# Kernel tuning notes

Hardware: AMD Instinct MI355X
Metric: run time of the kernel (lower is better)

## Reference

```python
import jax, jax.numpy as jnp
import numpy as np

N_NODES = 100000
N_EDGES = 3200000
# (out_dim, in_dim) for the 4 BayesianLinear layers: mlp1 = [5->16, 16->32], mlp2 = [35->16, 16->1]
LAYER_DIMS = [(16, 5), (32, 16), (16, 35), (1, 16)]


def setup_inputs() -> dict:
    key = jax.random.key(0)
    ks = iter(jax.random.split(key, 32))
    inp = {}
    inp["x"] = jax.random.normal(next(ks), (N_NODES, 3), jnp.float32)
    inp["edge_attr"] = jax.random.normal(next(ks), (N_EDGES, 2), jnp.float32)
    inp["edge_index"] = jax.random.randint(next(ks), (2, N_EDGES), 0, N_NODES, dtype=jnp.int64)
    for li, (o, i) in enumerate(LAYER_DIMS, 1):
        inp[f"l{li}_wmu"] = jax.random.normal(next(ks), (o, i), jnp.float32) * 0.1
        inp[f"l{li}_wrho"] = jax.random.normal(next(ks), (o, i), jnp.float32) * 0.1 - 5.0
        inp[f"l{li}_bmu"] = jax.random.normal(next(ks), (o,), jnp.float32) * 0.1
        inp[f"l{li}_brho"] = jax.random.normal(next(ks), (o,), jnp.float32) * 0.1 - 5.0
        inp[f"l{li}_eps_w"] = jax.random.normal(next(ks), (o, i), jnp.float32)
        inp[f"l{li}_eps_b"] = jax.random.normal(next(ks), (o,), jnp.float32)
    return inp


def _bayes_linear(h, wmu, wrho, bmu, brho, eps_w, eps_b):
    # sampled weight: W = mu + softplus(rho) * eps  (blitz BayesianLinear)
    W = wmu + jax.nn.softplus(wrho) * eps_w          # [out, in]
    b = bmu + jax.nn.softplus(brho) * eps_b          # [out]
    return h @ W.T + b


def _igconv(x, edge_index, edge_attr, p1, p2, p3, p4):
    src, dst = edge_index[0], edge_index[1]          # x_j = x[src], aggregate at dst
    x_j = x[src]                                     # [E, 3] irregular gather
    m = jnp.concatenate([x_j, edge_attr], axis=1)    # [E, 5]
    m = jax.nn.relu(_bayes_linear(m, *p1))           # [E, 16]
    m = jax.nn.relu(_bayes_linear(m, *p2))           # [E, 32]
    agg = jax.ops.segment_max(m, dst, num_segments=x.shape[0])  # [N, 32]
    agg = jnp.where(jnp.isneginf(agg), 0.0, agg)     # nodes with no in-edges -> 0
    h = jnp.concatenate([x, agg], axis=1)            # [N, 35]
    h = jax.nn.relu(_bayes_linear(h, *p3))           # [N, 16]
    comb = jax.nn.sigmoid(_bayes_linear(h, *p4))     # [N, 1]
    return jnp.concatenate([x[:, :2], comb], axis=1) # [N, 3]


def reference(x, edge_attr, edge_index,
              l1_wmu, l1_wrho, l1_bmu, l1_brho, l1_eps_w, l1_eps_b,
              l2_wmu, l2_wrho, l2_bmu, l2_brho, l2_eps_w, l2_eps_b,
              l3_wmu, l3_wrho, l3_bmu, l3_brho, l3_eps_w, l3_eps_b,
              l4_wmu, l4_wrho, l4_bmu, l4_brho, l4_eps_w, l4_eps_b):
    p1 = (l1_wmu, l1_wrho, l1_bmu, l1_brho, l1_eps_w, l1_eps_b)
    p2 = (l2_wmu, l2_wrho, l2_bmu, l2_brho, l2_eps_w, l2_eps_b)
    p3 = (l3_wmu, l3_wrho, l3_bmu, l3_brho, l3_eps_w, l3_eps_b)
    p4 = (l4_wmu, l4_wrho, l4_bmu, l4_brho, l4_eps_w, l4_eps_b)
    h = x
    for _ in range(3):  # three stacked applications of the same IGConv
        h = _igconv(h, edge_index, edge_attr, p1, p2, p3, p4)
    return h
```

## Files before the change

kernel.cpp:

```cpp
#include <hip/hip_runtime.h>
#include <math.h>

#define WTOT  1233
#define PKOFS 1280
#define PKTOT 352

typedef __fp16 h2 __attribute__((ext_vector_type(2)));
typedef __fp16 f16x8 __attribute__((ext_vector_type(8)));
typedef float f32x16 __attribute__((ext_vector_type(16)));

struct ERec { int s; int d; unsigned int ea; };

__device__ __forceinline__ h2 u2h(unsigned int u) { return __builtin_bit_cast(h2, u); }
__device__ __forceinline__ unsigned int h2u(h2 h) { return __builtin_bit_cast(unsigned int, h); }
#define DOT2(a, b, c) __builtin_amdgcn_fdot2((a), (b), (c), false)

__device__ __forceinline__ float softplus_f(float x) {
  return fmaxf(x, 0.f) + log1pf(expf(-fabsf(x)));
}

struct PrepArgs {
  const float* wmu[4]; const float* wrho[4]; const float* epsw[4];
  const float* bmu[4]; const float* brho[4]; const float* epsb[4];
  float* out; int* bucketCur; int nbuck;
};

__global__ void prep_all_kernel(PrepArgs a) {
  const int wsz[4] = {80, 512, 560, 16};
  const int wof[4] = {0, 96, 640, 1216};
  const int bsz[4] = {16, 32, 16, 1};
  const int bof[4] = {80, 608, 1200, 1232};
  float* wg = a.out;
  int tid = threadIdx.x;
  if (tid < a.nbuck) a.bucketCur[tid] = 0;
#pragma unroll
  for (int l = 0; l < 4; l++) {
    for (int i = tid; i < wsz[l]; i += 1024)
      wg[wof[l] + i] = a.wmu[l][i] + softplus_f(a.wrho[l][i]) * a.epsw[l][i];
    for (int i = tid; i < bsz[l]; i += 1024)
      wg[bof[l] + i] = a.bmu[l][i] + softplus_f(a.brho[l][i]) * a.epsb[l][i];
  }
  __syncthreads();
  unsigned int* wp = (unsigned int*)(wg + PKOFS);
  int t = tid;
  if (t < 16) {
    wp[t]      = h2u(h2{(__fp16)wg[t * 5 + 0], (__fp16)wg[t * 5 + 1]});
    wp[16 + t] = h2u(h2{(__fp16)wg[t * 5 + 2], (__fp16)0.f});
    wp[32 + t] = h2u(h2{(__fp16)wg[t * 5 + 3], (__fp16)wg[t * 5 + 4]});
    ((float*)wp)[304 + t] = wg[80 + t];
  }
  if (t < 32) {
    ((float*)wp)[320 + t] = wg[608 + t];
    for (int j = 0; j < 8; j++)
      wp[48 + t * 8 + j] =
          h2u(h2{(__fp16)wg[96 + t * 16 + 2 * j], (__fp16)wg[96 + t * 16 + 2 * j + 1]});
  }
}

__global__ __launch_bounds__(1024) void bhist_kernel(const int* __restrict__ dst,
                                                     int* __restrict__ bucketCur,
                                                     int E, int NBUCK) {
  __shared__ int h[1024];
  int tid = threadIdx.x;
  for (int i = tid; i < NBUCK; i += 1024) h[i] = 0;
  __syncthreads();
  int base = blockIdx.x * 8192;
#pragma unroll
  for (int r = 0; r < 8; r++) {
    int e = base + r * 1024 + tid;
    if (e < E) atomicAdd(&h[dst[e] >> 7], 1);
  }
  __syncthreads();
  for (int i = tid; i < NBUCK; i += 1024) {
    int c = h[i];
    if (c) atomicAdd(&bucketCur[i], c);
  }
}

__global__ __launch_bounds__(1024) void scanBk_kernel(int* __restrict__ bucketCur,
                                                      int* __restrict__ bucketOff,
                                                      int NBUCK) {
  __shared__ int wsum[16];
  __shared__ int woff[16];
  int tid = threadIdx.x, lane = tid & 63, wid = tid >> 6;
  int v = (tid < NBUCK) ? bucketCur[tid] : 0;
  int x = v;
#pragma unroll
  for (int off = 1; off < 64; off <<= 1) {
    int t = __shfl_up(x, off, 64);
    if (lane >= off) x += t;
  }
  if (lane == 63) wsum[wid] = x;
  __syncthreads();
  if (wid == 0) {
    int s = (lane < 16) ? wsum[lane] : 0;
#pragma unroll
    for (int off = 1; off < 16; off <<= 1) {
      int t = __shfl_up(s, off, 64);
      if (lane >= off) s += t;
    }
    if (lane < 16) woff[lane] = s - wsum[lane];
  }
  __syncthreads();
  int excl = woff[wid] + x - v;
  if (tid < NBUCK) {
    bucketOff[tid] = excl;
    bucketCur[tid] = excl;
    if (tid == NBUCK - 1) bucketOff[NBUCK] = excl + v;
  }
}

__global__ __launch_bounds__(1024) void part_kernel(
    const int* __restrict__ src, const int* __restrict__ dst,
    const float2* __restrict__ ea, int* __restrict__ bucketCur,
    ERec* __restrict__ brec, int E, int NBUCK) {
  __shared__ int h[1024];
  int tid = threadIdx.x;
  for (int i = tid; i < NBUCK; i += 1024) h[i] = 0;
  __syncthreads();
  int base = blockIdx.x * 8192;
  int d[8], s[8];
  unsigned int a[8];
  bool v[8];
#pragma unroll
  for (int j = 0; j < 8; j++) {
    int e = base + j * 1024 + tid;
    v[j] = e < E;
    if (v[j]) {
      d[j] = dst[e];
      s[j] = src[e];
      float2 t = ea[e];
      a[j] = h2u(__builtin_amdgcn_cvt_pkrtz(t.x, t.y));
      atomicAdd(&h[d[j] >> 7], 1);
    }
  }
  __syncthreads();
  for (int i = tid; i < NBUCK; i += 1024) {
    int c = h[i];
    h[i] = c ? atomicAdd(&bucketCur[i], c) : 0;
  }
  __syncthreads();
#pragma unroll
  for (int j = 0; j < 8; j++) {
    if (v[j]) {
      int pos = atomicAdd(&h[d[j] >> 7], 1);
      ERec t; t.s = s[j]; t.d = d[j]; t.ea = a[j];
      brec[pos] = t;
    }
  }
}

__global__ __launch_bounds__(256) void deg_kernel(const ERec* __restrict__ brec,
                                                  const int* __restrict__ bucketOff,
                                                  int* __restrict__ deg, int N) {
  __shared__ int cnt[128];
  int b = blockIdx.x, tid = threadIdx.x;
  if (tid < 128) cnt[tid] = 0;
  __syncthreads();
  int e0 = bucketOff[b], e1 = bucketOff[b + 1];
  for (int i = e0 + tid; i < e1; i += 256) atomicAdd(&cnt[brec[i].d & 127], 1);
  __syncthreads();
  int node = b * 128 + tid;
  if (tid < 128 && node < N) deg[node] = cnt[tid];
}

__global__ void scanA_kernel(const int* __restrict__ deg, int* __restrict__ part, int n) {
  __shared__ int ws[16];
  int tid = threadIdx.x;
  int i = blockIdx.x * 1024 + tid;
  int v = 0;
  if (i < n) v = (deg[i] + 3) & ~3;
#pragma unroll
  for (int off = 32; off >= 1; off >>= 1) v += __shfl_down(v, off, 64);
  if ((tid & 63) == 0) ws[tid >> 6] = v;
  __syncthreads();
  if (tid == 0) {
    int s = 0;
#pragma unroll
    for (int k = 0; k < 16; k++) s += ws[k];
    part[blockIdx.x] = s;
  }
}

__global__ void scanB_kernel(int* __restrict__ part, int P, int* __restrict__ etot) {
  int lane = threadIdx.x;
  int carry = 0;
  for (int base = 0; base < P; base += 64) {
    int i = base + lane;
    int v = (i < P) ? part[i] : 0;
    int x = v;
#pragma unroll
    for (int off = 1; off < 64; off <<= 1) {
      int t = __shfl_up(x, off, 64);
      if (lane >= off) x += t;
    }
    if (i < P) part[i] = carry + x - v;
    carry += __shfl(x, 63, 64);
  }
  if (lane == 0) *etot = carry;
}

__global__ void scanC_kernel(const int* __restrict__ deg, const int* __restrict__ part,
                             int* __restrict__ cursor, int n) {
  __shared__ int wsum[16];
  __shared__ int woff[16];
  int tid = threadIdx.x, lane = tid & 63, wid = tid >> 6;
  int i = blockIdx.x * 1024 + tid;
  int v = 0;
  if (i < n) v = (deg[i] + 3) & ~3;
  int x = v;
#pragma unroll
  for (int off = 1; off < 64; off <<= 1) {
    int t = __shfl_up(x, off, 64);
    if (lane >= off) x += t;
  }
  if (lane == 63) wsum[wid] = x;
  __syncthreads();
  if (wid == 0) {
    int s = (lane < 16) ? wsum[lane] : 0;
#pragma unroll
    for (int off = 1; off < 16; off <<= 1) {
      int t = __shfl_up(s, off, 64);
      if (lane >= off) s += t;
    }
    if (lane < 16) woff[lane] = s - wsum[lane];
  }
  __syncthreads();
  if (i < n) cursor[i] = part[blockIdx.x] + woff[wid] + x - v;
}

__global__ __launch_bounds__(256) void scat_kernel(
    const ERec* __restrict__ brec, const int* __restrict__ bucketOff,
    const int* __restrict__ cursor, ERec* __restrict__ erec, int N) {
  __shared__ int lcur[128];
  int b = blockIdx.x, tid = threadIdx.x;
  int node = b * 128 + tid;
  if (tid < 128) lcur[tid] = (node < N) ? cursor[node] : 0;
  __syncthreads();
  int e0 = bucketOff[b], e1 = bucketOff[b + 1];
  for (int i = e0 + tid; i < e1; i += 256) {
    ERec t = brec[i];
    int pos = atomicAdd(&lcur[t.d & 127], 1);
    erec[pos] = t;
  }
  __syncthreads();
  if (tid < 128 && node < N) {
    int cur = cursor[node];
    int endR = lcur[tid];
    int endP = cur + ((endR - cur + 3) & ~3);
    if (endR > cur) {
      ERec rep = erec[cur];
      for (int k = endR; k < endP; k++) erec[k] = rep;
    }
  }
}

__global__ void xpack_kernel(const float* __restrict__ x, uint2* __restrict__ xpk,
                             unsigned int* __restrict__ agg32, int n) {
  int i = blockIdx.x * blockDim.x + threadIdx.x;
  if (i < n) {
    h2 a = __builtin_amdgcn_cvt_pkrtz(x[3 * i], x[3 * i + 1]);
    h2 b = __builtin_amdgcn_cvt_pkrtz(x[3 * i + 2], 0.f);
    xpk[i] = make_uint2(h2u(a), h2u(b));
    uint4 z = make_uint4(0u, 0u, 0u, 0u);
    uint4* ap = (uint4*)(agg32 + (size_t)i * 32);
#pragma unroll
    for (int k = 0; k < 8; k++) ap[k] = z;
    if (i == 0) {
      uint4* as = (uint4*)(agg32 + (size_t)n * 32);
#pragma unroll
      for (int k = 0; k < 8; k++) as[k] = z;
    }
  }
}

__global__ __launch_bounds__(256) void edge_kernel(
    const uint2* __restrict__ xpk, const ERec* __restrict__ erec,
    unsigned int* __restrict__ agg32,
    const float* __restrict__ wg, const int* __restrict__ pEtot, int N) {
  __shared__ __align__(16) unsigned int lds[4][64][12];
  const unsigned int* wp = (const unsigned int*)(wg + PKOFS);
  const float* bf = (const float*)wp;
  const int Etot = *pEtot;
  if (blockIdx.x * 256 >= Etot) return;
  const int tid = threadIdx.x;
  const int lane = tid & 63;
  const int wslot = tid >> 6;
  const int e = blockIdx.x * 256 + tid;

  bool vld = e < Etot;
  ERec r;
  r.s = 0; r.d = N; r.ea = 0u;
  if (vld) r = erec[e];
  int d = r.d;
  uint2 xs = xpk[r.s];

  h2 p01 = u2h(xs.x), p2v = u2h(xs.y), pea = u2h(r.ea);
  unsigned int m1[8];
#pragma unroll
  for (int p = 0; p < 8; p++) {
    const int oA = 2 * p, oB = 2 * p + 1;
    float sA = DOT2(p01, u2h(wp[oA]),
                DOT2(p2v, u2h(wp[16 + oA]),
                DOT2(pea, u2h(wp[32 + oA]), bf[304 + oA])));
    float sB = DOT2(p01, u2h(wp[oB]),
                DOT2(p2v, u2h(wp[16 + oB]),
                DOT2(pea, u2h(wp[32 + oB]), bf[304 + oB])));
    m1[p] = h2u(__builtin_amdgcn_cvt_pkrtz(fmaxf(sA, 0.f), fmaxf(sB, 0.f)));
  }

  uint4* rowp = (uint4*)&lds[wslot][lane][0];
  rowp[0] = make_uint4(m1[0], m1[1], m1[2], m1[3]);
  rowp[1] = make_uint4(m1[4], m1[5], m1[6], m1[7]);
  asm volatile("s_waitcnt lgkmcnt(0)" ::: "memory");
  __builtin_amdgcn_sched_barrier(0);

  const int col = lane & 31;
  const int h = lane >> 5;
  f16x8 bfrag = __builtin_bit_cast(f16x8, *(const uint4*)&wp[48 + col * 8 + 4 * h]);
  float bias = bf[320 + col];
  f32x16 cini;
#pragma unroll
  for (int i = 0; i < 16; i++) cini[i] = bias;

  f16x8 a0 = __builtin_bit_cast(f16x8, *(const uint4*)&lds[wslot][col][4 * h]);
  f16x8 a1 = __builtin_bit_cast(f16x8, *(const uint4*)&lds[wslot][32 + col][4 * h]);
  f32x16 acc0 = __builtin_amdgcn_mfma_f32_32x32x16_f16(a0, bfrag, cini, 0, 0, 0);
  f32x16 acc1 = __builtin_amdgcn_mfma_f32_32x32x16_f16(a1, bfrag, cini, 0, 0, 0);

  float bm[2][4];
#pragma unroll
  for (int q = 0; q < 4; q++) {
    bm[0][q] = fmaxf(fmaxf(acc0[4 * q], acc0[4 * q + 1]),
                     fmaxf(acc0[4 * q + 2], fmaxf(acc0[4 * q + 3], 0.f)));
    bm[1][q] = fmaxf(fmaxf(acc1[4 * q], acc1[4 * q + 1]),
                     fmaxf(acc1[4 * q + 2], fmaxf(acc1[4 * q + 3], 0.f)));
  }

  int dp4 = __shfl_up(d, 4, 64);
  bool isHead = ((lane & 3) == 0) && (lane == 0 || d != dp4);
  unsigned long long hm = __ballot(isHead);

  unsigned long long rem = hm;
  while (rem) {
    int a = (int)__builtin_ctzll(rem);
    rem &= rem - 1;
    int b = rem ? (int)__builtin_ctzll(rem) : 64;
    int rd = __shfl(d, a, 64);
    int A = a >> 2, B = b >> 2;
    float mx = 0.f;
#pragma unroll
    for (int g = 0; g < 2; g++) {
#pragma unroll
      for (int q = 0; q < 4; q++) {
        int blk = 8 * g + 2 * q + h;
        bool in = (blk >= A) && (blk < B);
        mx = fmaxf(mx, in ? bm[g][q] : 0.f);
      }
    }
    mx = fmaxf(mx, __shfl_xor(mx, 32, 64));
    if (lane < 32 && rd < N)
      atomicMax(agg32 + (size_t)rd * 32 + col, __float_as_uint(mx));
  }
}

__global__ __launch_bounds__(256) void node_kernel(
    const float* __restrict__ x, const float* __restrict__ cin,
    float* __restrict__ cout, uint2* __restrict__ xpk,
    float* __restrict__ outFinal, unsigned int* __restrict__ agg32,
    const float* __restrict__ wg, int n) {
  int nid = blockIdx.x * blockDim.x + threadIdx.x;
  if (nid >= n) return;
  uint4* ap = (uint4*)(agg32 + (size_t)nid * 32);
  uint4 q[8];
#pragma unroll
  for (int i = 0; i < 8; i++) q[i] = ap[i];
  uint4 z = make_uint4(0u, 0u, 0u, 0u);
#pragma unroll
  for (int i = 0; i < 8; i++) ap[i] = z;
  float av[32];
#pragma unroll
  for (int i = 0; i < 8; i++) {
    av[4 * i + 0] = __uint_as_float(q[i].x);
    av[4 * i + 1] = __uint_as_float(q[i].y);
    av[4 * i + 2] = __uint_as_float(q[i].z);
    av[4 * i + 3] = __uint_as_float(q[i].w);
  }
  float x0 = x[3 * nid], x1 = x[3 * nid + 1];
  float x2 = cin ? cin[nid] : x[3 * nid + 2];
  float h[16];
#pragma unroll
  for (int o = 0; o < 16; o++) {
    float sa = wg[1200 + o];
    sa = fmaf(wg[640 + o * 35 + 0], x0, sa);
    sa = fmaf(wg[640 + o * 35 + 1], x1, sa);
    sa = fmaf(wg[640 + o * 35 + 2], x2, sa);
#pragma unroll
    for (int k = 0; k < 32; k++) sa = fmaf(wg[640 + o * 35 + 3 + k], av[k], sa);
    h[o] = fmaxf(sa, 0.f);
  }
  float z4 = wg[1232];
#pragma unroll
  for (int k = 0; k < 16; k++) z4 = fmaf(wg[1216 + k], h[k], z4);
  float comb = 1.f / (1.f + expf(-z4));
  cout[nid] = comb;
  ((unsigned int*)xpk)[2 * nid + 1] = h2u(__builtin_amdgcn_cvt_pkrtz(comb, 0.f));
  if (outFinal) {
    outFinal[3 * nid] = x0;
    outFinal[3 * nid + 1] = x1;
    outFinal[3 * nid + 2] = comb;
  }
}

extern "C" void kernel_launch(void* const* d_in, const int* in_sizes, int n_in,
                              void* d_out, int out_size, void* d_ws, size_t ws_size,
                              hipStream_t stream) {
  const float* x = (const float*)d_in[0];
  const float* ea = (const float*)d_in[1];
  const int* eidx = (const int*)d_in[2];
  const int N = in_sizes[0] / 3;
  const int E = in_sizes[1] / 2;
  const int* src = eidx;
  const int* dst = eidx + E;
  const int P = (N + 1023) / 1024;
  const int NBUCK = (N + 127) >> 7;
  const int EP = E + 3 * N;

  char* p = (char*)d_ws;
  size_t off = 0;
  auto alloc = [&](size_t bytes) -> char* {
    char* r = p + off;
    off = (off + bytes + 255) & ~(size_t)255;
    return r;
  };
  float* wbuf = (float*)alloc((size_t)(PKOFS + PKTOT) * 4);
  int* deg = (int*)alloc((size_t)N * 4);
  int* part = (int*)alloc((size_t)P * 4);
  int* cursor = (int*)alloc((size_t)N * 4);
  int* bucketOff = (int*)alloc(((size_t)NBUCK + 1) * 4);
  int* bucketCur = (int*)alloc((size_t)NBUCK * 4);
  int* etot = (int*)alloc(4);
  ERec* erec = (ERec*)alloc((size_t)EP * sizeof(ERec));
  char* uni = alloc((size_t)E * 12);
  ERec* brec = (ERec*)uni;
  size_t uoff = 0;
  auto ualloc = [&](size_t bytes) -> char* {
    char* r = uni + uoff;
    uoff = (uoff + bytes + 255) & ~(size_t)255;
    return r;
  };
  unsigned int* agg32 = (unsigned int*)ualloc(((size_t)N + 1) * 32 * 4);
  uint2* xpk = (uint2*)ualloc((size_t)N * 8);
  float* bufA = (float*)ualloc((size_t)N * 4);
  float* bufB = (float*)ualloc((size_t)N * 4);
  (void)ws_size;

  PrepArgs pa;
  for (int l = 0; l < 4; l++) {
    pa.wmu[l] = (const float*)d_in[3 + 6 * l + 0];
    pa.wrho[l] = (const float*)d_in[3 + 6 * l + 1];
    pa.bmu[l] = (const float*)d_in[3 + 6 * l + 2];
    pa.brho[l] = (const float*)d_in[3 + 6 * l + 3];
    pa.epsw[l] = (const float*)d_in[3 + 6 * l + 4];
    pa.epsb[l] = (const float*)d_in[3 + 6 * l + 5];
  }
  pa.out = wbuf;
  pa.bucketCur = bucketCur;
  pa.nbuck = NBUCK;

  const int TB = 256;
  auto blocks = [&](int n) { return dim3((n + TB - 1) / TB); };

  prep_all_kernel<<<dim3(1), dim3(1024), 0, stream>>>(pa);
  bhist_kernel<<<dim3((E + 8191) / 8192), dim3(1024), 0, stream>>>(dst, bucketCur, E, NBUCK);
  scanBk_kernel<<<dim3(1), dim3(1024), 0, stream>>>(bucketCur, bucketOff, NBUCK);
  part_kernel<<<dim3((E + 8191) / 8192), dim3(1024), 0, stream>>>(
      src, dst, (const float2*)ea, bucketCur, brec, E, NBUCK);
  deg_kernel<<<dim3(NBUCK), dim3(TB), 0, stream>>>(brec, bucketOff, deg, N);
  scanA_kernel<<<dim3(P), dim3(1024), 0, stream>>>(deg, part, N);
  scanB_kernel<<<dim3(1), dim3(64), 0, stream>>>(part, P, etot);
  scanC_kernel<<<dim3(P), dim3(1024), 0, stream>>>(deg, part, cursor, N);
  scat_kernel<<<dim3(NBUCK), dim3(TB), 0, stream>>>(brec, bucketOff, cursor, erec, N);
  xpack_kernel<<<blocks(N), dim3(TB), 0, stream>>>(x, xpk, agg32, N);

  float* outp = (float*)d_out;
  const int ebp = (EP + 255) / 256;
  edge_kernel<<<dim3(ebp), dim3(TB), 0, stream>>>(xpk, erec, agg32, wbuf, etot, N);
  node_kernel<<<blocks(N), dim3(TB), 0, stream>>>(x, nullptr, bufA, xpk, nullptr,
                                                  agg32, wbuf, N);
  edge_kernel<<<dim3(ebp), dim3(TB), 0, stream>>>(xpk, erec, agg32, wbuf, etot, N);
  node_kernel<<<blocks(N), dim3(TB), 0, stream>>>(x, bufA, bufB, xpk, nullptr,
                                                  agg32, wbuf, N);
  edge_kernel<<<dim3(ebp), dim3(TB), 0, stream>>>(xpk, erec, agg32, wbuf, etot, N);
  node_kernel<<<blocks(N), dim3(TB), 0, stream>>>(x, bufB, bufA, xpk, outp,
                                                  agg32, wbuf, N);
}
```

Measured before the change: 380.5 us.

## Process 128 edges per wave in edge kernel and widen dst buckets to 256 nodes

The edge kernel now has each wave handle two 64-edge groups, running four MFMA tiles per wave and merging head detection across the 128-edge span. Weight loads and the segment-max reduction loop are amortized over more edges, and the edge-kernel grid is halved. The node bucketing for the partition/degree/scatter passes is widened from 128 to 256 nodes per bucket, with 512-thread blocks, so there are fewer, larger buckets. In exchange the edge kernel uses more registers and LDS, which may lower occupancy, and the longer serial head loop may add divergence.

```diff
diff --git a/kernel.cpp b/kernel.cpp
--- a/kernel.cpp
+++ b/kernel.cpp
@@ -68,7 +68,7 @@
 #pragma unroll
   for (int r = 0; r < 8; r++) {
     int e = base + r * 1024 + tid;
-    if (e < E) atomicAdd(&h[dst[e] >> 7], 1);
+    if (e < E) atomicAdd(&h[dst[e] >> 8], 1);
   }
   __syncthreads();
   for (int i = tid; i < NBUCK; i += 1024) {
@@ -131,7 +131,7 @@
       s[j] = src[e];
       float2 t = ea[e];
       a[j] = h2u(__builtin_amdgcn_cvt_pkrtz(t.x, t.y));
-      atomicAdd(&h[d[j] >> 7], 1);
+      atomicAdd(&h[d[j] >> 8], 1);
     }
   }
   __syncthreads();
@@ -143,25 +143,25 @@
 #pragma unroll
   for (int j = 0; j < 8; j++) {
     if (v[j]) {
-      int pos = atomicAdd(&h[d[j] >> 7], 1);
+      int pos = atomicAdd(&h[d[j] >> 8], 1);
       ERec t; t.s = s[j]; t.d = d[j]; t.ea = a[j];
       brec[pos] = t;
     }
   }
 }
 
-__global__ __launch_bounds__(256) void deg_kernel(const ERec* __restrict__ brec,
+__global__ __launch_bounds__(512) void deg_kernel(const ERec* __restrict__ brec,
                                                   const int* __restrict__ bucketOff,
                                                   int* __restrict__ deg, int N) {
-  __shared__ int cnt[128];
+  __shared__ int cnt[256];
   int b = blockIdx.x, tid = threadIdx.x;
-  if (tid < 128) cnt[tid] = 0;
+  if (tid < 256) cnt[tid] = 0;
   __syncthreads();
   int e0 = bucketOff[b], e1 = bucketOff[b + 1];
-  for (int i = e0 + tid; i < e1; i += 256) atomicAdd(&cnt[brec[i].d & 127], 1);
-  __syncthreads();
-  int node = b * 128 + tid;
-  if (tid < 128 && node < N) deg[node] = cnt[tid];
+  for (int i = e0 + tid; i < e1; i += 512) atomicAdd(&cnt[brec[i].d & 255], 1);
+  __syncthreads();
+  int node = b * 256 + tid;
+  if (tid < 256 && node < N) deg[node] = cnt[tid];
 }
 
 __global__ void scanA_kernel(const int* __restrict__ deg, int* __restrict__ part, int n) {
@@ -229,22 +229,22 @@
   if (i < n) cursor[i] = part[blockIdx.x] + woff[wid] + x - v;
 }
 
-__global__ __launch_bounds__(256) void scat_kernel(
+__global__ __launch_bounds__(512) void scat_kernel(
     const ERec* __restrict__ brec, const int* __restrict__ bucketOff,
     const int* __restrict__ cursor, ERec* __restrict__ erec, int N) {
-  __shared__ int lcur[128];
+  __shared__ int lcur[256];
   int b = blockIdx.x, tid = threadIdx.x;
-  int node = b * 128 + tid;
-  if (tid < 128) lcur[tid] = (node < N) ? cursor[node] : 0;
+  int node = b * 256 + tid;
+  if (tid < 256) lcur[tid] = (node < N) ? cursor[node] : 0;
   __syncthreads();
   int e0 = bucketOff[b], e1 = bucketOff[b + 1];
-  for (int i = e0 + tid; i < e1; i += 256) {
+  for (int i = e0 + tid; i < e1; i += 512) {
     ERec t = brec[i];
-    int pos = atomicAdd(&lcur[t.d & 127], 1);
+    int pos = atomicAdd(&lcur[t.d & 255], 1);
     erec[pos] = t;
   }
   __syncthreads();
-  if (tid < 128 && node < N) {
+  if (tid < 256 && node < N) {
     int cur = cursor[node];
     int endR = lcur[tid];
     int endP = cur + ((endR - cur + 3) & ~3);
@@ -278,40 +278,48 @@
     const uint2* __restrict__ xpk, const ERec* __restrict__ erec,
     unsigned int* __restrict__ agg32,
     const float* __restrict__ wg, const int* __restrict__ pEtot, int N) {
-  __shared__ __align__(16) unsigned int lds[4][64][12];
+  __shared__ __align__(16) unsigned int lds[4][128][12];
   const unsigned int* wp = (const unsigned int*)(wg + PKOFS);
   const float* bf = (const float*)wp;
   const int Etot = *pEtot;
-  if (blockIdx.x * 256 >= Etot) return;
   const int tid = threadIdx.x;
   const int lane = tid & 63;
   const int wslot = tid >> 6;
-  const int e = blockIdx.x * 256 + tid;
-
-  bool vld = e < Etot;
-  ERec r;
-  r.s = 0; r.d = N; r.ea = 0u;
-  if (vld) r = erec[e];
-  int d = r.d;
-  uint2 xs = xpk[r.s];
-
-  h2 p01 = u2h(xs.x), p2v = u2h(xs.y), pea = u2h(r.ea);
-  unsigned int m1[8];
+  const int wbase = blockIdx.x * 512 + wslot * 128;
+  if (wbase >= Etot) return;
+
+  int e0 = wbase + lane, e1 = wbase + 64 + lane;
+  ERec r0, r1;
+  r0.s = 0; r0.d = N; r0.ea = 0u;
+  r1 = r0;
+  if (e0 < Etot) r0 = erec[e0];
+  if (e1 < Etot) r1 = erec[e1];
+  uint2 xs0 = xpk[r0.s];
+  uint2 xs1 = xpk[r1.s];
+
+  h2 p01a = u2h(xs0.x), p2va = u2h(xs0.y), peaa = u2h(r0.ea);
+  h2 p01b = u2h(xs1.x), p2vb = u2h(xs1.y), peab = u2h(r1.ea);
+  unsigned int m1a[8], m1b[8];
 #pragma unroll
   for (int p = 0; p < 8; p++) {
     const int oA = 2 * p, oB = 2 * p + 1;
-    float sA = DOT2(p01, u2h(wp[oA]),
-                DOT2(p2v, u2h(wp[16 + oA]),
-                DOT2(pea, u2h(wp[32 + oA]), bf[304 + oA])));
-    float sB = DOT2(p01, u2h(wp[oB]),
-                DOT2(p2v, u2h(wp[16 + oB]),
-                DOT2(pea, u2h(wp[32 + oB]), bf[304 + oB])));
-    m1[p] = h2u(__builtin_amdgcn_cvt_pkrtz(fmaxf(sA, 0.f), fmaxf(sB, 0.f)));
-  }
-
-  uint4* rowp = (uint4*)&lds[wslot][lane][0];
-  rowp[0] = make_uint4(m1[0], m1[1], m1[2], m1[3]);
-  rowp[1] = make_uint4(m1[4], m1[5], m1[6], m1[7]);
+    h2 wA0 = u2h(wp[oA]), wA1 = u2h(wp[16 + oA]), wA2 = u2h(wp[32 + oA]);
+    h2 wB0 = u2h(wp[oB]), wB1 = u2h(wp[16 + oB]), wB2 = u2h(wp[32 + oB]);
+    float bA = bf[304 + oA], bB = bf[304 + oB];
+    float sAa = DOT2(p01a, wA0, DOT2(p2va, wA1, DOT2(peaa, wA2, bA)));
+    float sBa = DOT2(p01a, wB0, DOT2(p2va, wB1, DOT2(peaa, wB2, bB)));
+    float sAb = DOT2(p01b, wA0, DOT2(p2vb, wA1, DOT2(peab, wA2, bA)));
+    float sBb = DOT2(p01b, wB0, DOT2(p2vb, wB1, DOT2(peab, wB2, bB)));
+    m1a[p] = h2u(__builtin_amdgcn_cvt_pkrtz(fmaxf(sAa, 0.f), fmaxf(sBa, 0.f)));
+    m1b[p] = h2u(__builtin_amdgcn_cvt_pkrtz(fmaxf(sAb, 0.f), fmaxf(sBb, 0.f)));
+  }
+
+  uint4* rp0 = (uint4*)&lds[wslot][lane][0];
+  rp0[0] = make_uint4(m1a[0], m1a[1], m1a[2], m1a[3]);
+  rp0[1] = make_uint4(m1a[4], m1a[5], m1a[6], m1a[7]);
+  uint4* rp1 = (uint4*)&lds[wslot][64 + lane][0];
+  rp1[0] = make_uint4(m1b[0], m1b[1], m1b[2], m1b[3]);
+  rp1[1] = make_uint4(m1b[4], m1b[5], m1b[6], m1b[7]);
   asm volatile("s_waitcnt lgkmcnt(0)" ::: "memory");
   __builtin_amdgcn_sched_barrier(0);
 
@@ -323,34 +331,37 @@
 #pragma unroll
   for (int i = 0; i < 16; i++) cini[i] = bias;
 
-  f16x8 a0 = __builtin_bit_cast(f16x8, *(const uint4*)&lds[wslot][col][4 * h]);
-  f16x8 a1 = __builtin_bit_cast(f16x8, *(const uint4*)&lds[wslot][32 + col][4 * h]);
-  f32x16 acc0 = __builtin_amdgcn_mfma_f32_32x32x16_f16(a0, bfrag, cini, 0, 0, 0);
-  f32x16 acc1 = __builtin_amdgcn_mfma_f32_32x32x16_f16(a1, bfrag, cini, 0, 0, 0);
-
-  float bm[2][4];
-#pragma unroll
-  for (int q = 0; q < 4; q++) {
-    bm[0][q] = fmaxf(fmaxf(acc0[4 * q], acc0[4 * q + 1]),
-                     fmaxf(acc0[4 * q + 2], fmaxf(acc0[4 * q + 3], 0.f)));
-    bm[1][q] = fmaxf(fmaxf(acc1[4 * q], acc1[4 * q + 1]),
-                     fmaxf(acc1[4 * q + 2], fmaxf(acc1[4 * q + 3], 0.f)));
-  }
-
-  int dp4 = __shfl_up(d, 4, 64);
-  bool isHead = ((lane & 3) == 0) && (lane == 0 || d != dp4);
-  unsigned long long hm = __ballot(isHead);
-
-  unsigned long long rem = hm;
-  while (rem) {
-    int a = (int)__builtin_ctzll(rem);
-    rem &= rem - 1;
-    int b = rem ? (int)__builtin_ctzll(rem) : 64;
-    int rd = __shfl(d, a, 64);
+  float bm[4][4];
+#pragma unroll
+  for (int g = 0; g < 4; g++) {
+    f16x8 a = __builtin_bit_cast(f16x8, *(const uint4*)&lds[wslot][32 * g + col][4 * h]);
+    f32x16 acc = __builtin_amdgcn_mfma_f32_32x32x16_f16(a, bfrag, cini, 0, 0, 0);
+#pragma unroll
+    for (int q = 0; q < 4; q++)
+      bm[g][q] = fmaxf(fmaxf(acc[4 * q], acc[4 * q + 1]),
+                       fmaxf(acc[4 * q + 2], fmaxf(acc[4 * q + 3], 0.f)));
+  }
+
+  int d0 = r0.d, d1 = r1.d;
+  int d0p4 = __shfl_up(d0, 4, 64);
+  int d1p4 = __shfl_up(d1, 4, 64);
+  int d0t = __shfl(d0, 60, 64);
+  bool head0 = ((lane & 3) == 0) && (lane == 0 || d0 != d0p4);
+  bool head1 = ((lane & 3) == 0) && (lane == 0 ? (d1 != d0t) : (d1 != d1p4));
+  unsigned long long m0 = __ballot(head0);
+  unsigned long long m1 = __ballot(head1);
+
+  while (m0 | m1) {
+    int a;
+    if (m0) { a = (int)__builtin_ctzll(m0); m0 &= m0 - 1; }
+    else    { a = 64 + (int)__builtin_ctzll(m1); m1 &= m1 - 1; }
+    int b = m0 ? (int)__builtin_ctzll(m0)
+               : (m1 ? 64 + (int)__builtin_ctzll(m1) : 128);
+    int rd = (a < 64) ? __shfl(d0, a, 64) : __shfl(d1, a - 64, 64);
     int A = a >> 2, B = b >> 2;
     float mx = 0.f;
 #pragma unroll
-    for (int g = 0; g < 2; g++) {
+    for (int g = 0; g < 4; g++) {
 #pragma unroll
       for (int q = 0; q < 4; q++) {
         int blk = 8 * g + 2 * q + h;
@@ -423,7 +434,7 @@
   const int* src = eidx;
   const int* dst = eidx + E;
   const int P = (N + 1023) / 1024;
-  const int NBUCK = (N + 127) >> 7;
+  const int NBUCK = (N + 255) >> 8;
   const int EP = E + 3 * N;
 
   char* p = (char*)d_ws;
@@ -476,15 +487,15 @@
   scanBk_kernel<<<dim3(1), dim3(1024), 0, stream>>>(bucketCur, bucketOff, NBUCK);
   part_kernel<<<dim3((E + 8191) / 8192), dim3(1024), 0, stream>>>(
       src, dst, (const float2*)ea, bucketCur, brec, E, NBUCK);
-  deg_kernel<<<dim3(NBUCK), dim3(TB), 0, stream>>>(brec, bucketOff, deg, N);
+  deg_kernel<<<dim3(NBUCK), dim3(512), 0, stream>>>(brec, bucketOff, deg, N);
   scanA_kernel<<<dim3(P), dim3(1024), 0, stream>>>(deg, part, N);
   scanB_kernel<<<dim3(1), dim3(64), 0, stream>>>(part, P, etot);
   scanC_kernel<<<dim3(P), dim3(1024), 0, stream>>>(deg, part, cursor, N);
-  scat_kernel<<<dim3(NBUCK), dim3(TB), 0, stream>>>(brec, bucketOff, cursor, erec, N);
+  scat_kernel<<<dim3(NBUCK), dim3(512), 0, stream>>>(brec, bucketOff, cursor, erec, N);
   xpack_kernel<<<blocks(N), dim3(TB), 0, stream>>>(x, xpk, agg32, N);
 
   float* outp = (float*)d_out;
-  const int ebp = (EP + 255) / 256;
+  const int ebp = (EP + 511) / 512;
   edge_kernel<<<dim3(ebp), dim3(TB), 0, stream>>>(xpk, erec, agg32, wbuf, etot, N);
   node_kernel<<<blocks(N), dim3(TB), 0, stream>>>(x, nullptr, bufA, xpk, nullptr,
                                                   agg32, wbuf, N);
```

After: 431.6 us. +13.4%, slower.
